# Kernel optimization log

Measured on AMD Instinct MI355X. Metric: run time of the kernel, lower is better.

## Reference

```python
import jax, jax.numpy as jnp
import numpy as np

TEMP = 1.0  # composition softmax temperature

def _bank_topk(x, U, V, logits, top_k):
    # softmax over primitive logits, select top-k, renormalize, fused low-rank projection
    w = jax.nn.softmax(logits / TEMP)                     # [P]
    tw, ti = jax.lax.top_k(w, top_k)                      # [k], [k]
    tw = tw / tw.sum()
    Us = U[ti]                                            # [k, d_in, r]
    Vs = V[ti]                                            # [k, r, d_out]
    h = jnp.einsum('bsd,kdr->bksr', x, Us)                # low-rank bottleneck
    return jnp.einsum('bksr,kro,k->bso', h, Vs, tw)       # weighted fuse

def reference(x, q_U, q_V, k_U, k_V, v_U, v_V, q_logits, k_logits, v_logits, out_w, top_k):
    B, S, _ = x.shape
    H, D = 16, 64
    q = _bank_topk(x, q_U, q_V, q_logits, top_k)
    k = _bank_topk(x, k_U, k_V, k_logits, top_k)
    v = _bank_topk(x, v_U, v_V, v_logits, top_k)
    q = q.reshape(B, S, H, D).transpose(0, 2, 1, 3)       # [B,H,S,D]
    k = k.reshape(B, S, H, D).transpose(0, 2, 1, 3)
    v = v.reshape(B, S, H, D).transpose(0, 2, 1, 3)
    scale = 1.0 / jnp.sqrt(jnp.asarray(D, dtype=x.dtype))
    scores = jnp.einsum('bhqd,bhkd->bhqk', q, k) * scale  # [B,H,S,S]
    causal = jnp.triu(jnp.ones((S, S), dtype=bool), 1)
    scores = jnp.where(causal[None, None], jnp.finfo(x.dtype).min, scores)
    probs = jax.nn.softmax(scores, axis=-1)
    out = jnp.einsum('bhqk,bhkd->bhqd', probs, v)
    out = out.transpose(0, 2, 1, 3).reshape(B, S, H * D)
    return out @ out_w.T                                   # nn.Linear(H*D, d_model, bias=False)

def setup_inputs() -> dict:
    key = jax.random.key(0)
    ks = jax.random.split(key, 11)
    P, d, r = 16, 1024, 64
    B, S = 4, 1024
    f = jnp.float32
    inp = {
        'x': jax.random.normal(ks[0], (B, S, d), f),
        'q_U': jax.random.normal(ks[1], (P, d, r), f) * (1.0 / np.sqrt(d)),
        'q_V': jax.random.normal(ks[2], (P, r, d), f) * (1.0 / np.sqrt(r)),
        'k_U': jax.random.normal(ks[3], (P, d, r), f) * (1.0 / np.sqrt(d)),
        'k_V': jax.random.normal(ks[4], (P, r, d), f) * (1.0 / np.sqrt(r)),
        'v_U': jax.random.normal(ks[5], (P, d, r), f) * (1.0 / np.sqrt(d)),
        'v_V': jax.random.normal(ks[6], (P, r, d), f) * (1.0 / np.sqrt(r)),
        'q_logits': jax.random.normal(ks[7], (P,), f) * 0.01,
        'k_logits': jax.random.normal(ks[8], (P,), f) * 0.01,
        'v_logits': jax.random.normal(ks[9], (P,), f) * 0.01,
        'out_w': jax.random.normal(ks[10], (d, d), f) * (1.0 / np.sqrt(d)),
        'top_k': 4,
    }
    return inp
```

## Files before the change

### kernel.cpp

```cpp
#include <hip/hip_runtime.h>
#include <math.h>

#define D_MODEL 1024
#define RANK    64
#define PMAX    16
#define S_LEN   1024
#define HD      64
#define MROWS   4096
#define NHEAD   16
#define BATCH   4

typedef short short8v __attribute__((ext_vector_type(8)));
typedef float floatx4 __attribute__((ext_vector_type(4)));

typedef __attribute__((address_space(1))) const unsigned int* gptr_t;
typedef __attribute__((address_space(3))) unsigned int* lptr_t;

static __device__ __forceinline__ void async16(const void* g, void* l) {
    __builtin_amdgcn_global_load_lds((gptr_t)g, (lptr_t)l, 16, 0, 0);
}

static __device__ __forceinline__ short f2bf(float f) {
    unsigned int u = __float_as_uint(f);
    u = (u + 0x7fffu + ((u >> 16) & 1u)) >> 16;
    return (short)u;
}

__global__ void topk_weights_kernel(const float* __restrict__ ql,
                                    const float* __restrict__ kl,
                                    const float* __restrict__ vl,
                                    const int* __restrict__ topk,
                                    int* __restrict__ idx_out,
                                    float* __restrict__ w_out) {
    int bank = threadIdx.x;
    if (bank >= 3) return;
    const float* lg = (bank == 0) ? ql : (bank == 1) ? kl : vl;
    int K = *topk; if (K < 1) K = 1; if (K > PMAX) K = PMAX;
    float l[PMAX];
    for (int i = 0; i < PMAX; ++i) l[i] = lg[i];
    bool used[PMAX];
    for (int i = 0; i < PMAX; ++i) used[i] = false;
    int   sel_i[PMAX];
    float sel_l[PMAX];
    for (int j = 0; j < K; ++j) {
        int best = -1; float bv = -INFINITY;
        for (int i = 0; i < PMAX; ++i)
            if (!used[i] && l[i] > bv) { bv = l[i]; best = i; }
        used[best] = true; sel_i[j] = best; sel_l[j] = bv;
    }
    float mx = sel_l[0];
    float e[PMAX];
    float sum = 0.f;
    for (int j = 0; j < K; ++j) { e[j] = __expf(sel_l[j] - mx); sum += e[j]; }
    float inv = 1.f / sum;
    for (int j = 0; j < PMAX; ++j) {
        idx_out[bank * PMAX + j] = (j < K) ? sel_i[j] : 0;
        w_out[bank * PMAX + j]   = (j < K) ? e[j] * inv : 0.f;
    }
}

__global__ __launch_bounds__(256) void convert_bf16_kernel(
    const float* __restrict__ src, short* __restrict__ dst, int n4) {
    int i = blockIdx.x * 256 + threadIdx.x;
    if (i < n4) {
        float4 f = ((const float4*)src)[i];
        short4 o;
        o.x = f2bf(f.x); o.y = f2bf(f.y); o.z = f2bf(f.z); o.w = f2bf(f.w);
        ((short4*)dst)[i] = o;
    }
}

__global__ __launch_bounds__(256) void prep_uv_kernel(
    const float* __restrict__ qU, const float* __restrict__ kU,
    const float* __restrict__ vU,
    const float* __restrict__ qV, const float* __restrict__ kV,
    const float* __restrict__ vV,
    const int* __restrict__ idx, const float* __restrict__ wsel,
    short* __restrict__ Ut, short* __restrict__ Vt) {
    int z    = blockIdx.z;
    int j    = blockIdx.y;
    int tile = blockIdx.x;
    int t    = threadIdx.x;
    __shared__ float T[64][65];
    int bank = (z < 3) ? z : z - 3;
    int p = idx[bank * PMAX + j];

    if (z < 3) {
        const float* U = (bank == 0) ? qU : (bank == 1) ? kU : vU;
        const float* src = U + (size_t)p * D_MODEL * RANK;
        int d0 = tile * 64;
        int rl = t & 63, dq = t >> 6;
#pragma unroll
        for (int i = 0; i < 16; ++i) {
            int dl = i * 4 + dq;
            T[rl][dl] = src[(size_t)(d0 + dl) * RANK + rl];
        }
        __syncthreads();
        short* dst = Ut + (size_t)bank * D_MODEL * D_MODEL;
        int rr = t >> 2;
#pragma unroll
        for (int i = 0; i < 4; ++i) {
            int c = (t & 3) * 16 + i * 4;
            short4 o;
            o.x = f2bf(T[rr][c + 0]); o.y = f2bf(T[rr][c + 1]);
            o.z = f2bf(T[rr][c + 2]); o.w = f2bf(T[rr][c + 3]);
            *(short4*)&dst[(size_t)(j * 64 + rr) * D_MODEL + d0 + c] = o;
        }
    } else {
        const float* V = (bank == 0) ? qV : (bank == 1) ? kV : vV;
        float wj = wsel[bank * PMAX + j];
        const float* src = V + (size_t)p * RANK * D_MODEL;
        int n0 = tile * 64;
        int nl = t & 63, rq = t >> 6;
#pragma unroll
        for (int i = 0; i < 16; ++i) {
            int rl = i * 4 + rq;
            T[nl][rl] = src[(size_t)rl * D_MODEL + n0 + nl] * wj;
        }
        __syncthreads();
        short* dst = Vt + (size_t)bank * D_MODEL * D_MODEL;
        int rr = t >> 2;
#pragma unroll
        for (int i = 0; i < 4; ++i) {
            int c = (t & 3) * 16 + i * 4;
            short4 o;
            o.x = f2bf(T[rr][c + 0]); o.y = f2bf(T[rr][c + 1]);
            o.z = f2bf(T[rr][c + 2]); o.w = f2bf(T[rr][c + 3]);
            *(short4*)&dst[(size_t)(n0 + rr) * D_MODEL + j * 64 + c] = o;
        }
    }
}

static __device__ __forceinline__ void mfma_gemm_tile(
    const short* __restrict__ A, const short* __restrict__ B, int kl,
    int m0, int n0, short* As, short* Bs, floatx4 acc[4][4]) {
    const int t    = threadIdx.x;
    const int w    = t >> 6;
    const int lane = t & 63;
    const int wm   = w & 1, wn = w >> 1;
    const int colL = lane & 15, quad = lane >> 4;
    const int srow  = lane >> 2;
    const int skoff = (lane & 3) * 8;

#pragma unroll
    for (int i = 0; i < 4; ++i)
#pragma unroll
        for (int j = 0; j < 4; ++j) acc[i][j] = (floatx4){0.f, 0.f, 0.f, 0.f};

    for (int k0 = 0; k0 < kl; k0 += 32) {
        async16(A + (size_t)(m0 + w * 16 + srow) * D_MODEL + k0 + skoff,
                As + (w * 16 + srow) * 32 + skoff);
        async16(A + (size_t)(m0 + 64 + w * 16 + srow) * D_MODEL + k0 + skoff,
                As + (64 + w * 16 + srow) * 32 + skoff);
        async16(B + (size_t)(n0 + w * 16 + srow) * D_MODEL + k0 + skoff,
                Bs + (w * 16 + srow) * 32 + skoff);
        async16(B + (size_t)(n0 + 64 + w * 16 + srow) * D_MODEL + k0 + skoff,
                Bs + (64 + w * 16 + srow) * 32 + skoff);
        __syncthreads();
        short8v af[4], bf[4];
#pragma unroll
        for (int i = 0; i < 4; ++i)
            af[i] = *(const short8v*)&As[(wm * 64 + i * 16 + colL) * 32 + quad * 8];
#pragma unroll
        for (int j = 0; j < 4; ++j)
            bf[j] = *(const short8v*)&Bs[(wn * 64 + j * 16 + colL) * 32 + quad * 8];
#pragma unroll
        for (int i = 0; i < 4; ++i)
#pragma unroll
            for (int j = 0; j < 4; ++j)
                acc[i][j] = __builtin_amdgcn_mfma_f32_16x16x32_bf16(af[i], bf[j], acc[i][j], 0, 0, 0);
        __syncthreads();
    }
}

__global__ __launch_bounds__(256) void gemm_h_kernel(
    const short* __restrict__ xb, const short* __restrict__ Ut,
    const int* __restrict__ topk, short* __restrict__ h) {
    int K = *topk; if (K < 1) K = 1; if (K > PMAX) K = PMAX;
    int n0 = blockIdx.y * 128;
    if (n0 >= K * 64) return;
    int m0 = blockIdx.x * 128;
    int bank = blockIdx.z;
    __shared__ short As[128 * 32];
    __shared__ short Bs[128 * 32];
    floatx4 acc[4][4];
    mfma_gemm_tile(xb, Ut + (size_t)bank * D_MODEL * D_MODEL, D_MODEL, m0, n0, As, Bs, acc);

    const int t = threadIdx.x, w = t >> 6, lane = t & 63;
    const int wm = w & 1, wn = w >> 1, colL = lane & 15, quad = lane >> 4;
    short* H = h + (size_t)bank * MROWS * D_MODEL;
#pragma unroll
    for (int i = 0; i < 4; ++i)
#pragma unroll
        for (int j = 0; j < 4; ++j)
#pragma unroll
            for (int r = 0; r < 4; ++r)
                H[(size_t)(m0 + wm * 64 + i * 16 + quad * 4 + r) * D_MODEL +
                  (n0 + wn * 64 + j * 16 + colL)] = f2bf(acc[i][j][r]);
}

__global__ __launch_bounds__(256) void gemm_qkv_kernel(
    const short* __restrict__ h, const short* __restrict__ Vt,
    const int* __restrict__ topk, short* __restrict__ qkv) {
    int K = *topk; if (K < 1) K = 1; if (K > PMAX) K = PMAX;
    int m0 = blockIdx.x * 128;
    int n0 = blockIdx.y * 128;
    int bank = blockIdx.z;
    __shared__ short As[128 * 32];
    __shared__ short Bs[128 * 32];
    floatx4 acc[4][4];
    mfma_gemm_tile(h + (size_t)bank * MROWS * D_MODEL,
                   Vt + (size_t)bank * D_MODEL * D_MODEL, K * 64, m0, n0, As, Bs, acc);

    const int t = threadIdx.x, w = t >> 6, lane = t & 63;
    const int wm = w & 1, wn = w >> 1, colL = lane & 15, quad = lane >> 4;
    short* outp = qkv + (size_t)bank * MROWS * D_MODEL;
#pragma unroll
    for (int i = 0; i < 4; ++i)
#pragma unroll
        for (int j = 0; j < 4; ++j)
#pragma unroll
            for (int r = 0; r < 4; ++r) {
                int m = m0 + wm * 64 + i * 16 + quad * 4 + r;
                int n = n0 + wn * 64 + j * 16 + colL;
                int b = m >> 10, s = m & 1023;
                int head = n >> 6, d = n & 63;
                outp[(((size_t)(b * NHEAD + head) << 10) + s) * HD + d] = f2bf(acc[i][j][r]);
            }
}

__global__ __launch_bounds__(256) void gemm_proj_kernel(
    const short* __restrict__ attnb, const short* __restrict__ wb,
    float* __restrict__ outp) {
    int m0 = blockIdx.x * 128;
    int n0 = blockIdx.y * 128;
    __shared__ short As[128 * 32];
    __shared__ short Bs[128 * 32];
    floatx4 acc[4][4];
    mfma_gemm_tile(attnb, wb, D_MODEL, m0, n0, As, Bs, acc);

    const int t = threadIdx.x, w = t >> 6, lane = t & 63;
    const int wm = w & 1, wn = w >> 1, colL = lane & 15, quad = lane >> 4;
#pragma unroll
    for (int i = 0; i < 4; ++i)
#pragma unroll
        for (int j = 0; j < 4; ++j)
#pragma unroll
            for (int r = 0; r < 4; ++r)
                outp[(size_t)(m0 + wm * 64 + i * 16 + quad * 4 + r) * D_MODEL +
                     (n0 + wn * 64 + j * 16 + colL)] = acc[i][j][r];
}

__global__ __launch_bounds__(256) void attn_mfma_kernel(
    const short* __restrict__ qkv,
    short* __restrict__ attn_out) {
    const int t    = threadIdx.x;
    const int w    = t >> 6;
    const int lane = t & 63;
    const int col  = lane & 15;
    const int quad = lane >> 4;
    const int pr   = blockIdx.x;
    const int bh   = blockIdx.y;
    const size_t HS   = (size_t)S_LEN * HD;
    const size_t BSTR = (size_t)MROWS * D_MODEL;
    const short* Qg = qkv + (size_t)bh * HS;
    const short* Kg = qkv + BSTR + (size_t)bh * HS;
    const short* Vg = qkv + 2 * BSTR + (size_t)bh * HS;

    __shared__ short Ks[64][72];
    __shared__ short Vt[64][72];
    __shared__ short Ps[4][16][72];

    const float SC = 0.125f * 1.44269504f;

    for (int ph = 0; ph < 2; ++ph) {
        const int qt = ph ? (15 - pr) : pr;
        const int qrow = qt * 64 + w * 16 + col;
        short8v aq0 = *(const short8v*)(Qg + (size_t)qrow * HD + quad * 8);
        short8v aq1 = *(const short8v*)(Qg + (size_t)qrow * HD + 32 + quad * 8);
        floatx4 O0 = {0.f, 0.f, 0.f, 0.f}, O1 = O0, O2 = O0, O3 = O0;
        float mrow[4] = {-INFINITY, -INFINITY, -INFINITY, -INFINITY};
        float lrow[4] = {0.f, 0.f, 0.f, 0.f};

        for (int jt = 0; jt <= qt; ++jt) {
            __syncthreads();
            {
                int c = t;
                int key = c >> 3, db = (c & 7) * 8;
                *(short8v*)&Ks[key][db] =
                    *(const short8v*)(Kg + (size_t)(jt * 64 + key) * HD + db);
                c = t + 256;
                key = c >> 3; db = (c & 7) * 8;
                *(short8v*)&Ks[key][db] =
                    *(const short8v*)(Kg + (size_t)(jt * 64 + key) * HD + db);
            }
            {
                int k0 = (t & 31) * 2;
                int db = (t >> 5) * 8;
                short8v v0 = *(const short8v*)(Vg + (size_t)(jt * 64 + k0) * HD + db);
                short8v v1 = *(const short8v*)(Vg + (size_t)(jt * 64 + k0 + 1) * HD + db);
#pragma unroll
                for (int i = 0; i < 8; ++i) {
                    unsigned int pk = (unsigned int)(unsigned short)v0[i] |
                                      ((unsigned int)(unsigned short)v1[i] << 16);
                    *(unsigned int*)&Vt[db + i][k0] = pk;
                }
            }
            __syncthreads();

            const bool diag = (jt == qt);
            const int  nmax = diag ? w : 3;
            float sc[4][4];
#pragma unroll
            for (int n = 0; n < 4; ++n) {
                if (n <= nmax) {
                    floatx4 c4 = {0.f, 0.f, 0.f, 0.f};
                    short8v b0 = *(const short8v*)&Ks[n * 16 + col][quad * 8];
                    short8v b1 = *(const short8v*)&Ks[n * 16 + col][32 + quad * 8];
                    c4 = __builtin_amdgcn_mfma_f32_16x16x32_bf16(aq0, b0, c4, 0, 0, 0);
                    c4 = __builtin_amdgcn_mfma_f32_16x16x32_bf16(aq1, b1, c4, 0, 0, 0);
#pragma unroll
                    for (int r = 0; r < 4; ++r) {
                        float v = c4[r] * SC;
                        if (diag && n == w && col > quad * 4 + r) v = -INFINITY;
                        sc[n][r] = v;
                    }
                } else {
#pragma unroll
                    for (int r = 0; r < 4; ++r) sc[n][r] = -INFINITY;
                }
            }
            float pv[4][4];
#pragma unroll
            for (int r = 0; r < 4; ++r) {
                float tm = fmaxf(fmaxf(sc[0][r], sc[1][r]), fmaxf(sc[2][r], sc[3][r]));
                tm = fmaxf(tm, __shfl_xor(tm, 1));
                tm = fmaxf(tm, __shfl_xor(tm, 2));
                tm = fmaxf(tm, __shfl_xor(tm, 4));
                tm = fmaxf(tm, __shfl_xor(tm, 8));
                float mnew  = fmaxf(mrow[r], tm);
                float alpha = exp2f(mrow[r] - mnew);
                float ps = 0.f;
#pragma unroll
                for (int n = 0; n < 4; ++n) {
                    float p = exp2f(sc[n][r] - mnew);
                    pv[n][r] = p;
                    ps += p;
                }
                ps += __shfl_xor(ps, 1);
                ps += __shfl_xor(ps, 2);
                ps += __shfl_xor(ps, 4);
                ps += __shfl_xor(ps, 8);
                lrow[r] = lrow[r] * alpha + ps;
                mrow[r] = mnew;
                O0[r] *= alpha; O1[r] *= alpha; O2[r] *= alpha; O3[r] *= alpha;
            }
#pragma unroll
            for (int n = 0; n < 4; ++n)
#pragma unroll
                for (int r = 0; r < 4; ++r)
                    Ps[w][quad * 4 + r][n * 16 + col] = f2bf(pv[n][r]);
            const int ksmax = diag ? (w >> 1) : 1;
#pragma unroll
            for (int ks = 0; ks < 2; ++ks) {
                if (ks > ksmax) break;
                short8v ap  = *(const short8v*)&Ps[w][col][ks * 32 + quad * 8];
                short8v bv0 = *(const short8v*)&Vt[0  + col][ks * 32 + quad * 8];
                short8v bv1 = *(const short8v*)&Vt[16 + col][ks * 32 + quad * 8];
                short8v bv2 = *(const short8v*)&Vt[32 + col][ks * 32 + quad * 8];
                short8v bv3 = *(const short8v*)&Vt[48 + col][ks * 32 + quad * 8];
                O0 = __builtin_amdgcn_mfma_f32_16x16x32_bf16(ap, bv0, O0, 0, 0, 0);
                O1 = __builtin_amdgcn_mfma_f32_16x16x32_bf16(ap, bv1, O1, 0, 0, 0);
                O2 = __builtin_amdgcn_mfma_f32_16x16x32_bf16(ap, bv2, O2, 0, 0, 0);
                O3 = __builtin_amdgcn_mfma_f32_16x16x32_bf16(ap, bv3, O3, 0, 0, 0);
            }
        }
        const int b  = bh >> 4;
        const int hh = bh & 15;
        short* orow = attn_out +
            ((size_t)(b * S_LEN) + qt * 64 + w * 16) * D_MODEL + hh * 64;
#pragma unroll
        for (int r = 0; r < 4; ++r) {
            float inv = 1.f / lrow[r];
            short* prw = orow + (size_t)(quad * 4 + r) * D_MODEL;
            prw[0  + col] = f2bf(O0[r] * inv);
            prw[16 + col] = f2bf(O1[r] * inv);
            prw[32 + col] = f2bf(O2[r] * inv);
            prw[48 + col] = f2bf(O3[r] * inv);
        }
    }
}

extern "C" void kernel_launch(void* const* d_in, const int* in_sizes, int n_in,
                              void* d_out, int out_size, void* d_ws, size_t ws_size,
                              hipStream_t stream) {
    const float* x    = (const float*)d_in[0];
    const float* qU   = (const float*)d_in[1];
    const float* qV   = (const float*)d_in[2];
    const float* kU   = (const float*)d_in[3];
    const float* kV   = (const float*)d_in[4];
    const float* vU   = (const float*)d_in[5];
    const float* vV   = (const float*)d_in[6];
    const float* qlg  = (const float*)d_in[7];
    const float* klg  = (const float*)d_in[8];
    const float* vlg  = (const float*)d_in[9];
    const float* outw = (const float*)d_in[10];
    const int*   topk = (const int*)d_in[11];
    float* outp = (float*)d_out;

    char* ws = (char*)d_ws;
    int*   idxp = (int*)ws;
    float* wp   = (float*)(ws + 256);
    short* xb   = (short*)(ws + 512);
    short* Ut   = xb + (size_t)MROWS * D_MODEL;
    short* Vt   = Ut + (size_t)3 * D_MODEL * D_MODEL;
    short* wb   = Vt + (size_t)3 * D_MODEL * D_MODEL;
    short* hbuf = wb + (size_t)D_MODEL * D_MODEL;
    short* qkvb = hbuf + (size_t)3 * MROWS * D_MODEL;
    short* attnb = qkvb + (size_t)3 * MROWS * D_MODEL;

    topk_weights_kernel<<<1, 64, 0, stream>>>(qlg, klg, vlg, topk, idxp, wp);
    convert_bf16_kernel<<<(MROWS * D_MODEL / 4 + 255) / 256, 256, 0, stream>>>(
        x, xb, MROWS * D_MODEL / 4);
    convert_bf16_kernel<<<(D_MODEL * D_MODEL / 4 + 255) / 256, 256, 0, stream>>>(
        outw, wb, D_MODEL * D_MODEL / 4);
    prep_uv_kernel<<<dim3(16, 16, 6), 256, 0, stream>>>(
        qU, kU, vU, qV, kV, vV, idxp, wp, Ut, Vt);
    gemm_h_kernel<<<dim3(32, 8, 3), 256, 0, stream>>>(xb, Ut, topk, hbuf);
    gemm_qkv_kernel<<<dim3(32, 8, 3), 256, 0, stream>>>(hbuf, Vt, topk, qkvb);
    attn_mfma_kernel<<<dim3(8, 64), 256, 0, stream>>>(qkvb, attnb);
    gemm_proj_kernel<<<dim3(32, 8), 256, 0, stream>>>(attnb, wb, outp);
}
```

Baseline: 230.7 us.

## Double-buffer attention K/V tiles with async LDS loads and pre-transposed V

Restructures the attention kernel to prefetch the next K/V tile into a second LDS buffer using async global-to-LDS loads, overlapping those loads with compute, and uses XOR-swizzled LDS layouts to avoid bank conflicts. V is transposed once by a new kernel rather than per tile inside attention, and the softmax scale is folded into the Q projection epilogue. Row-sum shuffles are deferred to the end of the loop. This adds an extra kernel launch and workspace buffer, and folding the scale into bf16 Q changes rounding slightly.

```diff
diff --git a/kernel.cpp b/kernel.cpp
--- a/kernel.cpp
+++ b/kernel.cpp
@@ -215,6 +215,7 @@
     const int t = threadIdx.x, w = t >> 6, lane = t & 63;
     const int wm = w & 1, wn = w >> 1, colL = lane & 15, quad = lane >> 4;
     short* outp = qkv + (size_t)bank * MROWS * D_MODEL;
+    const float scl = (bank == 0) ? 0.18033688f : 1.0f;
 #pragma unroll
     for (int i = 0; i < 4; ++i)
 #pragma unroll
@@ -225,34 +226,108 @@
                 int n = n0 + wn * 64 + j * 16 + colL;
                 int b = m >> 10, s = m & 1023;
                 int head = n >> 6, d = n & 63;
-                outp[(((size_t)(b * NHEAD + head) << 10) + s) * HD + d] = f2bf(acc[i][j][r]);
+                outp[(((size_t)(b * NHEAD + head) << 10) + s) * HD + d] = f2bf(acc[i][j][r] * scl);
             }
 }
 
-__global__ __launch_bounds__(256) void gemm_proj_kernel(
-    const short* __restrict__ attnb, const short* __restrict__ wb,
-    float* __restrict__ outp) {
-    int m0 = blockIdx.x * 128;
-    int n0 = blockIdx.y * 128;
-    __shared__ short As[128 * 32];
-    __shared__ short Bs[128 * 32];
-    floatx4 acc[4][4];
-    mfma_gemm_tile(attnb, wb, D_MODEL, m0, n0, As, Bs, acc);
-
-    const int t = threadIdx.x, w = t >> 6, lane = t & 63;
-    const int wm = w & 1, wn = w >> 1, colL = lane & 15, quad = lane >> 4;
-#pragma unroll
-    for (int i = 0; i < 4; ++i)
-#pragma unroll
-        for (int j = 0; j < 4; ++j)
-#pragma unroll
-            for (int r = 0; r < 4; ++r)
-                outp[(size_t)(m0 + wm * 64 + i * 16 + quad * 4 + r) * D_MODEL +
-                     (n0 + wn * 64 + j * 16 + colL)] = acc[i][j][r];
+__global__ __launch_bounds__(256) void transpose_v_kernel(
+    const short* __restrict__ src, short* __restrict__ dst) {
+    int st = blockIdx.x, bh = blockIdx.y;
+    __shared__ short T[64][72];
+    const short* S = src + (size_t)bh * (S_LEN * HD) + (size_t)st * 64 * HD;
+    int r = threadIdx.x >> 2, i = threadIdx.x & 3;
+    *(short8v*)&T[r][i * 16]     = *(const short8v*)&S[r * HD + i * 16];
+    *(short8v*)&T[r][i * 16 + 8] = *(const short8v*)&S[r * HD + i * 16 + 8];
+    __syncthreads();
+    short* Drow = dst + (size_t)bh * (S_LEN * HD) + (size_t)r * S_LEN + st * 64 + i * 16;
+    short8v o0, o1;
+#pragma unroll
+    for (int k = 0; k < 8; ++k) o0[k] = T[i * 16 + k][r];
+#pragma unroll
+    for (int k = 0; k < 8; ++k) o1[k] = T[i * 16 + 8 + k][r];
+    *(short8v*)&Drow[0] = o0;
+    *(short8v*)&Drow[8] = o1;
+}
+
+static __device__ __forceinline__ void stage_tiles(
+    const short* __restrict__ Kg, const short* __restrict__ Vg, int jt,
+    short* KsB, short* VsB, int w, int lane) {
+#pragma unroll
+    for (int q = 0; q < 2; ++q) {
+        int c   = q * 64 + lane;
+        int r16 = c >> 3;
+        int i   = c & 7;
+        int r   = w * 16 + r16;
+        int g   = i ^ (r16 & 7);
+        async16(Kg + (size_t)(jt * 64 + r) * HD + g * 8, KsB + r * 64 + i * 8);
+        async16(Vg + (size_t)r * S_LEN + jt * 64 + g * 8, VsB + r * 64 + i * 8);
+    }
+}
+
+template<bool DIAG>
+static __device__ __forceinline__ void attn_step(
+    const short* KsB, const short* VsB, short* Pw,
+    short8v aq0, short8v aq1, int w, int col, int quad,
+    floatx4& O0, floatx4& O1, floatx4& O2, floatx4& O3,
+    float mrow[4], float lrow[4]) {
+    const int colLow = col & 7;
+    floatx4 c4[4];
+#pragma unroll
+    for (int n = 0; n < 4; ++n) {
+        if (!DIAG || n <= w) {
+            floatx4 z = {0.f, 0.f, 0.f, 0.f};
+            short8v b0 = *(const short8v*)&KsB[(n * 16 + col) * 64 + ((quad ^ colLow) << 3)];
+            short8v b1 = *(const short8v*)&KsB[(n * 16 + col) * 64 + (((quad + 4) ^ colLow) << 3)];
+            z = __builtin_amdgcn_mfma_f32_16x16x32_bf16(aq0, b0, z, 0, 0, 0);
+            z = __builtin_amdgcn_mfma_f32_16x16x32_bf16(aq1, b1, z, 0, 0, 0);
+            if (DIAG) {
+#pragma unroll
+                for (int r = 0; r < 4; ++r)
+                    if (n == w && col > quad * 4 + r) z[r] = -INFINITY;
+            }
+            c4[n] = z;
+        } else {
+            c4[n] = (floatx4){-INFINITY, -INFINITY, -INFINITY, -INFINITY};
+        }
+    }
+#pragma unroll
+    for (int r = 0; r < 4; ++r) {
+        float tm = fmaxf(fmaxf(c4[0][r], c4[1][r]), fmaxf(c4[2][r], c4[3][r]));
+        tm = fmaxf(tm, __shfl_xor(tm, 1));
+        tm = fmaxf(tm, __shfl_xor(tm, 2));
+        tm = fmaxf(tm, __shfl_xor(tm, 4));
+        tm = fmaxf(tm, __shfl_xor(tm, 8));
+        float mnew  = fmaxf(mrow[r], tm);
+        float alpha = exp2f(mrow[r] - mnew);
+        float p0 = exp2f(c4[0][r] - mnew), p1 = exp2f(c4[1][r] - mnew);
+        float p2 = exp2f(c4[2][r] - mnew), p3 = exp2f(c4[3][r] - mnew);
+        lrow[r] = lrow[r] * alpha + (p0 + p1 + p2 + p3);
+        mrow[r] = mnew;
+        O0[r] *= alpha; O1[r] *= alpha; O2[r] *= alpha; O3[r] *= alpha;
+        short* pr = Pw + (quad * 4 + r) * 72 + col;
+        pr[0]  = f2bf(p0); pr[16] = f2bf(p1);
+        pr[32] = f2bf(p2); pr[48] = f2bf(p3);
+    }
+    const int ksmax = DIAG ? (w >> 1) : 1;
+#pragma unroll
+    for (int ks = 0; ks < 2; ++ks) {
+        if (ks > ksmax) break;
+        short8v ap = *(const short8v*)&Pw[col * 72 + ks * 32 + quad * 8];
+        int pc = ((ks * 4 + quad) ^ colLow) << 3;
+        short8v v0 = *(const short8v*)&VsB[(0  + col) * 64 + pc];
+        short8v v1 = *(const short8v*)&VsB[(16 + col) * 64 + pc];
+        short8v v2 = *(const short8v*)&VsB[(32 + col) * 64 + pc];
+        short8v v3 = *(const short8v*)&VsB[(48 + col) * 64 + pc];
+        O0 = __builtin_amdgcn_mfma_f32_16x16x32_bf16(ap, v0, O0, 0, 0, 0);
+        O1 = __builtin_amdgcn_mfma_f32_16x16x32_bf16(ap, v1, O1, 0, 0, 0);
+        O2 = __builtin_amdgcn_mfma_f32_16x16x32_bf16(ap, v2, O2, 0, 0, 0);
+        O3 = __builtin_amdgcn_mfma_f32_16x16x32_bf16(ap, v3, O3, 0, 0, 0);
+    }
 }
 
 __global__ __launch_bounds__(256) void attn_mfma_kernel(
     const short* __restrict__ qkv,
+    const short* __restrict__ vtb,
     short* __restrict__ attn_out) {
     const int t    = threadIdx.x;
     const int w    = t >> 6;
@@ -265,13 +340,12 @@
     const size_t BSTR = (size_t)MROWS * D_MODEL;
     const short* Qg = qkv + (size_t)bh * HS;
     const short* Kg = qkv + BSTR + (size_t)bh * HS;
-    const short* Vg = qkv + 2 * BSTR + (size_t)bh * HS;
-
-    __shared__ short Ks[64][72];
-    __shared__ short Vt[64][72];
-    __shared__ short Ps[4][16][72];
-
-    const float SC = 0.125f * 1.44269504f;
+    const short* Vg = vtb + (size_t)bh * HS;
+
+    __shared__ short Ks[2][4096];
+    __shared__ short Vs[2][4096];
+    __shared__ short Ps[4][16 * 72];
+    short* Pw = &Ps[w][0];
 
     for (int ph = 0; ph < 2; ++ph) {
         const int qt = ph ? (15 - pr) : pr;
@@ -282,106 +356,30 @@
         float mrow[4] = {-INFINITY, -INFINITY, -INFINITY, -INFINITY};
         float lrow[4] = {0.f, 0.f, 0.f, 0.f};
 
-        for (int jt = 0; jt <= qt; ++jt) {
+        __syncthreads();
+        stage_tiles(Kg, Vg, 0, Ks[0], Vs[0], w, lane);
+        __syncthreads();
+        int cur = 0;
+        for (int jt = 0; jt < qt; ++jt) {
+            stage_tiles(Kg, Vg, jt + 1, Ks[cur ^ 1], Vs[cur ^ 1], w, lane);
+            attn_step<false>(Ks[cur], Vs[cur], Pw, aq0, aq1, w, col, quad,
+                             O0, O1, O2, O3, mrow, lrow);
             __syncthreads();
-            {
-                int c = t;
-                int key = c >> 3, db = (c & 7) * 8;
-                *(short8v*)&Ks[key][db] =
-                    *(const short8v*)(Kg + (size_t)(jt * 64 + key) * HD + db);
-                c = t + 256;
-                key = c >> 3; db = (c & 7) * 8;
-                *(short8v*)&Ks[key][db] =
-                    *(const short8v*)(Kg + (size_t)(jt * 64 + key) * HD + db);
-            }
-            {
-                int k0 = (t & 31) * 2;
-                int db = (t >> 5) * 8;
-                short8v v0 = *(const short8v*)(Vg + (size_t)(jt * 64 + k0) * HD + db);
-                short8v v1 = *(const short8v*)(Vg + (size_t)(jt * 64 + k0 + 1) * HD + db);
-#pragma unroll
-                for (int i = 0; i < 8; ++i) {
-                    unsigned int pk = (unsigned int)(unsigned short)v0[i] |
-                                      ((unsigned int)(unsigned short)v1[i] << 16);
-                    *(unsigned int*)&Vt[db + i][k0] = pk;
-                }
-            }
-            __syncthreads();
-
-            const bool diag = (jt == qt);
-            const int  nmax = diag ? w : 3;
-            float sc[4][4];
-#pragma unroll
-            for (int n = 0; n < 4; ++n) {
-                if (n <= nmax) {
-                    floatx4 c4 = {0.f, 0.f, 0.f, 0.f};
-                    short8v b0 = *(const short8v*)&Ks[n * 16 + col][quad * 8];
-                    short8v b1 = *(const short8v*)&Ks[n * 16 + col][32 + quad * 8];
-                    c4 = __builtin_amdgcn_mfma_f32_16x16x32_bf16(aq0, b0, c4, 0, 0, 0);
-                    c4 = __builtin_amdgcn_mfma_f32_16x16x32_bf16(aq1, b1, c4, 0, 0, 0);
-#pragma unroll
-                    for (int r = 0; r < 4; ++r) {
-                        float v = c4[r] * SC;
-                        if (diag && n == w && col > quad * 4 + r) v = -INFINITY;
-                        sc[n][r] = v;
-                    }
-                } else {
-#pragma unroll
-                    for (int r = 0; r < 4; ++r) sc[n][r] = -INFINITY;
-                }
-            }
-            float pv[4][4];
-#pragma unroll
-            for (int r = 0; r < 4; ++r) {
-                float tm = fmaxf(fmaxf(sc[0][r], sc[1][r]), fmaxf(sc[2][r], sc[3][r]));
-                tm = fmaxf(tm, __shfl_xor(tm, 1));
-                tm = fmaxf(tm, __shfl_xor(tm, 2));
-                tm = fmaxf(tm, __shfl_xor(tm, 4));
-                tm = fmaxf(tm, __shfl_xor(tm, 8));
-                float mnew  = fmaxf(mrow[r], tm);
-                float alpha = exp2f(mrow[r] - mnew);
-                float ps = 0.f;
-#pragma unroll
-                for (int n = 0; n < 4; ++n) {
-                    float p = exp2f(sc[n][r] - mnew);
-                    pv[n][r] = p;
-                    ps += p;
-                }
-                ps += __shfl_xor(ps, 1);
-                ps += __shfl_xor(ps, 2);
-                ps += __shfl_xor(ps, 4);
-                ps += __shfl_xor(ps, 8);
-                lrow[r] = lrow[r] * alpha + ps;
-                mrow[r] = mnew;
-                O0[r] *= alpha; O1[r] *= alpha; O2[r] *= alpha; O3[r] *= alpha;
-            }
-#pragma unroll
-            for (int n = 0; n < 4; ++n)
-#pragma unroll
-                for (int r = 0; r < 4; ++r)
-                    Ps[w][quad * 4 + r][n * 16 + col] = f2bf(pv[n][r]);
-            const int ksmax = diag ? (w >> 1) : 1;
-#pragma unroll
-            for (int ks = 0; ks < 2; ++ks) {
-                if (ks > ksmax) break;
-                short8v ap  = *(const short8v*)&Ps[w][col][ks * 32 + quad * 8];
-                short8v bv0 = *(const short8v*)&Vt[0  + col][ks * 32 + quad * 8];
-                short8v bv1 = *(const short8v*)&Vt[16 + col][ks * 32 + quad * 8];
-                short8v bv2 = *(const short8v*)&Vt[32 + col][ks * 32 + quad * 8];
-                short8v bv3 = *(const short8v*)&Vt[48 + col][ks * 32 + quad * 8];
-                O0 = __builtin_amdgcn_mfma_f32_16x16x32_bf16(ap, bv0, O0, 0, 0, 0);
-                O1 = __builtin_amdgcn_mfma_f32_16x16x32_bf16(ap, bv1, O1, 0, 0, 0);
-                O2 = __builtin_amdgcn_mfma_f32_16x16x32_bf16(ap, bv2, O2, 0, 0, 0);
-                O3 = __builtin_amdgcn_mfma_f32_16x16x32_bf16(ap, bv3, O3, 0, 0, 0);
-            }
-        }
+            cur ^= 1;
+        }
+        attn_step<true>(Ks[cur], Vs[cur], Pw, aq0, aq1, w, col, quad,
+                        O0, O1, O2, O3, mrow, lrow);
+
         const int b  = bh >> 4;
         const int hh = bh & 15;
         short* orow = attn_out +
             ((size_t)(b * S_LEN) + qt * 64 + w * 16) * D_MODEL + hh * 64;
 #pragma unroll
         for (int r = 0; r < 4; ++r) {
-            float inv = 1.f / lrow[r];
+            float l = lrow[r];
+            l += __shfl_xor(l, 1); l += __shfl_xor(l, 2);
+            l += __shfl_xor(l, 4); l += __shfl_xor(l, 8);
+            float inv = 1.f / l;
             short* prw = orow + (size_t)(quad * 4 + r) * D_MODEL;
             prw[0  + col] = f2bf(O0[r] * inv);
             prw[16 + col] = f2bf(O1[r] * inv);
@@ -389,6 +387,28 @@
             prw[48 + col] = f2bf(O3[r] * inv);
         }
     }
+}
+
+__global__ __launch_bounds__(256) void gemm_proj_kernel(
+    const short* __restrict__ attnb, const short* __restrict__ wb,
+    float* __restrict__ outp) {
+    int m0 = blockIdx.x * 128;
+    int n0 = blockIdx.y * 128;
+    __shared__ short As[128 * 32];
+    __shared__ short Bs[128 * 32];
+    floatx4 acc[4][4];
+    mfma_gemm_tile(attnb, wb, D_MODEL, m0, n0, As, Bs, acc);
+
+    const int t = threadIdx.x, w = t >> 6, lane = t & 63;
+    const int wm = w & 1, wn = w >> 1, colL = lane & 15, quad = lane >> 4;
+#pragma unroll
+    for (int i = 0; i < 4; ++i)
+#pragma unroll
+        for (int j = 0; j < 4; ++j)
+#pragma unroll
+            for (int r = 0; r < 4; ++r)
+                outp[(size_t)(m0 + wm * 64 + i * 16 + quad * 4 + r) * D_MODEL +
+                     (n0 + wn * 64 + j * 16 + colL)] = acc[i][j][r];
 }
 
 extern "C" void kernel_launch(void* const* d_in, const int* in_sizes, int n_in,
@@ -418,6 +438,7 @@
     short* hbuf = wb + (size_t)D_MODEL * D_MODEL;
     short* qkvb = hbuf + (size_t)3 * MROWS * D_MODEL;
     short* attnb = qkvb + (size_t)3 * MROWS * D_MODEL;
+    short* vtb  = attnb + (size_t)MROWS * D_MODEL;
 
     topk_weights_kernel<<<1, 64, 0, stream>>>(qlg, klg, vlg, topk, idxp, wp);
     convert_bf16_kernel<<<(MROWS * D_MODEL / 4 + 255) / 256, 256, 0, stream>>>(
@@ -428,6 +449,8 @@
         qU, kU, vU, qV, kV, vV, idxp, wp, Ut, Vt);
     gemm_h_kernel<<<dim3(32, 8, 3), 256, 0, stream>>>(xb, Ut, topk, hbuf);
     gemm_qkv_kernel<<<dim3(32, 8, 3), 256, 0, stream>>>(hbuf, Vt, topk, qkvb);
-    attn_mfma_kernel<<<dim3(8, 64), 256, 0, stream>>>(qkvb, attnb);
+    transpose_v_kernel<<<dim3(16, 64), 256, 0, stream>>>(
+        qkvb + (size_t)2 * MROWS * D_MODEL, vtb);
+    attn_mfma_kernel<<<dim3(8, 64), 256, 0, stream>>>(qkvb, vtb, attnb);
     gemm_proj_kernel<<<dim3(32, 8), 256, 0, stream>>>(attnb, wb, outp);
 }
```

Measured after the change: 231.3 us. No clear change (+0.3%).
